# Optimization experiments

Hardware: AMD Instinct MI355X
Metric: run time of the kernel (lower is better)

The kernel has to match this reference:

```python
import jax, jax.numpy as jnp
import numpy as np

N_USERS = 100000
N_ITEMS = 50000
N_NODES = N_USERS + N_ITEMS  # 150000
N_EDGES = 1000000
N_INTENTS = 4
EMBED_K = 64
CHUNK = EMBED_K // N_INTENTS  # 16
N_LAYERS = 3


def setup_inputs() -> dict:
    key = jax.random.key(0)
    k1, k2, k3, k4 = jax.random.split(key, 4)
    Gu = jax.random.normal(k1, (N_USERS, EMBED_K), dtype=jnp.float32) * 0.1
    Gi = jax.random.normal(k2, (N_ITEMS, EMBED_K), dtype=jnp.float32) * 0.1
    edge_index = jax.random.randint(k3, (2, N_EDGES), 0, N_NODES, dtype=jnp.int64)
    edge_index_intents = jax.random.normal(k4, (N_INTENTS, N_EDGES), dtype=jnp.float32)
    return {"Gu": Gu, "Gi": Gi, "edge_index": edge_index,
            "edge_index_intents": edge_index_intents}


def dgcf_layer(x, row, col, edge_index_intents):
    # x: [N, K, C]; edge_index_intents: [K, E]
    w = jax.nn.softmax(edge_index_intents, axis=0).T  # [E, K]
    deg = (jax.ops.segment_sum(w, row, num_segments=N_NODES)
           + jax.ops.segment_sum(w, col, num_segments=N_NODES))  # [N, K]
    # deg^-0.5 with inf -> 0 (as in the torch code)
    dis = jnp.where(deg > 0, 1.0 / jnp.sqrt(jnp.maximum(deg, 1e-12)), 0.0)  # [N, K]
    norm = dis[row] * dis[col]  # [E, K]
    msg = norm[:, :, None] * x[row]  # [E, K, C] gather-multiply
    return jax.ops.segment_sum(msg, col, num_segments=N_NODES)  # scatter-add at targets


def reference(Gu, Gi, edge_index, edge_index_intents):
    row, col = edge_index[0], edge_index[1]
    # ego embeddings split into intent chunks: [N, K, C]
    x = jnp.concatenate([Gu, Gi], axis=0).reshape(N_NODES, N_INTENTS, CHUNK)
    for _ in range(N_LAYERS):
        x = dgcf_layer(x, row, col, edge_index_intents)
    return x
```

## Files before the change

### kernel.cpp

```cpp
#include <hip/hip_runtime.h>
#include <hip/hip_bf16.h>
#include <hip/hip_fp16.h>
#include <math.h>

#define N_USERS 100000
#define N_ITEMS 50000
#define N_NODES 150000
#define N_EDGES 1000000
#define N_GU_FLAT (N_USERS * 64)
#define N_ALL_FLAT (N_NODES * 64)
#define NBUCK 586
#define HPITCH (2 * NBUCK)
#define EPB 4096
#define NEB ((N_EDGES + EPB - 1) / EPB)
#define BCAP 2048
#define FIXS 16777216.0f
#define GCAST ((N_ALL_FLAT / 4 + 1023) / 1024)

typedef __hip_bfloat16 bf16;
typedef unsigned short ushort_t;
typedef unsigned int uint_t;
typedef unsigned long long u64_t;

__device__ __forceinline__ ushort_t f2bs(float f) {
    bf16 h = __float2bfloat16(f);
    return *reinterpret_cast<ushort_t*>(&h);
}
__device__ __forceinline__ float lo2f(uint_t u) {
    float f; *reinterpret_cast<uint_t*>(&f) = u << 16; return f;
}
__device__ __forceinline__ float hi2f(uint_t u) {
    float f; *reinterpret_cast<uint_t*>(&f) = u & 0xFFFF0000u; return f;
}
__device__ __forceinline__ uint_t pack2(float a, float b) {
    return (uint_t)f2bs(a) | ((uint_t)f2bs(b) << 16);
}
__device__ __forceinline__ ushort_t f2hs(float f) {
    __half h = __float2half(f);
    return *reinterpret_cast<ushort_t*>(&h);
}
__device__ __forceinline__ float hs2f(ushort_t u) {
    __half h; *reinterpret_cast<ushort_t*>(&h) = u;
    return __half2float(h);
}
__device__ __forceinline__ int fix24(float w) {
    return (int)__float2int_rn(w * FIXS);
}

__global__ __launch_bounds__(1024) void s3_scatter(
        const int* __restrict__ ei, const float* __restrict__ intents,
        uint_t* __restrict__ gctr,
        uint_t* __restrict__ tmp_meta, u64_t* __restrict__ tmp_w,
        u64_t* __restrict__ tmp_row) {
    extern __shared__ char smem[];
    u64_t*  cw    = (u64_t*)smem;
    u64_t*  rw    = (u64_t*)(smem + 32768);
    uint_t* cmeta = (uint_t*)(smem + 65536);
    uint_t* cpos  = (uint_t*)(smem + 81920);
    uint_t* rpos  = (uint_t*)(smem + 98304);
    uint_t* ctr   = (uint_t*)(smem + 114688);
    uint_t* lexcl = (uint_t*)(smem + 119376);
    uint_t* gb    = (uint_t*)(smem + 124064);
    uint_t* stmp  = cpos;
    int b = blockIdx.x, t = threadIdx.x;
    for (int j = t; j < HPITCH; j += 1024) ctr[j] = 0;
    __syncthreads();
    int eb = b * EPB;
    int lim = min(EPB, N_EDGES - eb);
    int  jcol[4], jrow[4];
    uint_t rkc[4], rkr[4], meta[4];
    u64_t cwv[4], rwv[4];
    bool val[4];
#pragma unroll
    for (int q = 0; q < 4; ++q) {
        int i = t + q * 1024;
        val[q] = (i < lim);
        int e = eb + (val[q] ? i : 0);
        int r = ei[e];
        int c = ei[N_EDGES + e];
        float v0 = intents[e];
        float v1 = intents[N_EDGES + e];
        float v2 = intents[2 * N_EDGES + e];
        float v3 = intents[3 * N_EDGES + e];
        float m  = fmaxf(fmaxf(v0, v1), fmaxf(v2, v3));
        float x0 = __expf(v0 - m), x1 = __expf(v1 - m);
        float x2 = __expf(v2 - m), x3 = __expf(v3 - m);
        float inv = 1.0f / (x0 + x1 + x2 + x3);
        float w0 = x0 * inv, w1 = x1 * inv, w2 = x2 * inv, w3 = x3 * inv;
        jcol[q] = c >> 8;
        jrow[q] = r >> 8;
        if (val[q]) {
            rkc[q] = atomicAdd(&ctr[jcol[q]], 1u);
            rkr[q] = atomicAdd(&ctr[NBUCK + jrow[q]], 1u);
        }
        meta[q] = ((uint_t)(c & 255) << 24) | (uint_t)r;
        cwv[q]  = (u64_t)pack2(w0, w1) | ((u64_t)pack2(w2, w3) << 32);
        rwv[q]  = (u64_t)f2hs(w0) | ((u64_t)f2hs(w1) << 16) |
                  ((u64_t)f2hs(w2) << 32) | ((u64_t)(uint_t)(r & 255) << 48);
    }
    __syncthreads();
    for (int j = t; j < HPITCH; j += 1024)
        gb[j] = atomicAdd(&gctr[j], ctr[j]);
    {
        uint_t v = (t < NBUCK) ? ctr[t] : 0u;
        stmp[t] = v;
        __syncthreads();
        for (int off = 1; off < 1024; off <<= 1) {
            uint_t a = (t >= off) ? stmp[t - off] : 0u;
            __syncthreads();
            stmp[t] += a;
            __syncthreads();
        }
        if (t < NBUCK) lexcl[t] = stmp[t] - v;
    }
    __syncthreads();
    {
        uint_t v = (t < NBUCK) ? ctr[NBUCK + t] : 0u;
        stmp[t] = v;
        __syncthreads();
        for (int off = 1; off < 1024; off <<= 1) {
            uint_t a = (t >= off) ? stmp[t - off] : 0u;
            __syncthreads();
            stmp[t] += a;
            __syncthreads();
        }
        if (t < NBUCK) lexcl[NBUCK + t] = stmp[t] - v;
    }
    __syncthreads();
#pragma unroll
    for (int q = 0; q < 4; ++q) {
        if (!val[q]) continue;
        uint_t lp = lexcl[jcol[q]] + rkc[q];
        cmeta[lp] = meta[q];
        cw[lp]    = cwv[q];
        cpos[lp]  = (uint_t)jcol[q] * BCAP + gb[jcol[q]] + rkc[q];
        uint_t lr = lexcl[NBUCK + jrow[q]] + rkr[q];
        rw[lr]    = rwv[q];
        rpos[lr]  = (uint_t)jrow[q] * BCAP + gb[NBUCK + jrow[q]] + rkr[q];
    }
    __syncthreads();
    for (int i = t; i < lim; i += 1024) {
        uint_t p = cpos[i];
        tmp_meta[p] = cmeta[i];
        tmp_w[p]    = cw[i];
        tmp_row[rpos[i]] = rw[i];
    }
}

__global__ __launch_bounds__(1024) void s4_finalize(
        const uint_t* __restrict__ tmp_meta, const u64_t* __restrict__ tmp_w,
        const u64_t* __restrict__ tmp_row, const uint_t* __restrict__ gctr,
        const float* __restrict__ Gu, const float* __restrict__ Gi,
        ushort_t* __restrict__ xG,
        uint_t* __restrict__ rec_src, int* __restrict__ offs_c, int* __restrict__ cnt_c,
        float* __restrict__ dis) {
    __shared__ uint_t meta_s[BCAP];
    __shared__ u64_t  w_s[BCAP];
    __shared__ u64_t  rw_s[BCAP];
    __shared__ uint_t hist[256], excl[256], run[256], sc[256];
    __shared__ int deg[1024];
    int b = blockIdx.x, t = threadIdx.x;
    if (b >= NBUCK) {
        long base = ((long)(b - NBUCK) * 1024 + t) * 4;
        if (base >= N_ALL_FLAT) return;
        float4 v = (base < N_GU_FLAT) ? *(const float4*)(Gu + base)
                                      : *(const float4*)(Gi + (base - N_GU_FLAT));
        uint2 o;
        o.x = pack2(v.x, v.y);
        o.y = pack2(v.z, v.w);
        *(uint2*)(xG + base) = o;
        return;
    }
    if (t < 256) { hist[t] = 0u; run[t] = 0u; }
    deg[t] = 0;
    __syncthreads();
    uint_t c0 = (uint_t)b * BCAP;
    int nc = min((int)gctr[b], BCAP);
    int nr = min((int)gctr[NBUCK + b], BCAP);
    for (int i = t; i < nc; i += 1024) {
        meta_s[i] = tmp_meta[c0 + i];
        w_s[i]    = tmp_w[c0 + i];
    }
    for (int i = t; i < nr; i += 1024) rw_s[i] = tmp_row[c0 + i];
    __syncthreads();
    for (int i = t; i < nc; i += 1024) {
        uint_t nl = meta_s[i] >> 24;
        u64_t w = w_s[i];
        atomicAdd(&hist[nl], 1u);
        atomicAdd(&deg[nl * 4 + 0], fix24(lo2f((uint_t)w)));
        atomicAdd(&deg[nl * 4 + 1], fix24(hi2f((uint_t)w)));
        atomicAdd(&deg[nl * 4 + 2], fix24(lo2f((uint_t)(w >> 32))));
        atomicAdd(&deg[nl * 4 + 3], fix24(hi2f((uint_t)(w >> 32))));
    }
    for (int i = t; i < nr; i += 1024) {
        u64_t rv = rw_s[i];
        uint_t nl = (uint_t)(rv >> 48) & 255u;
        float w0 = hs2f((ushort_t)(rv & 0xFFFF));
        float w1 = hs2f((ushort_t)((rv >> 16) & 0xFFFF));
        float w2 = hs2f((ushort_t)((rv >> 32) & 0xFFFF));
        float w3 = 1.0f - w0 - w1 - w2;
        atomicAdd(&deg[nl * 4 + 0], fix24(w0));
        atomicAdd(&deg[nl * 4 + 1], fix24(w1));
        atomicAdd(&deg[nl * 4 + 2], fix24(w2));
        atomicAdd(&deg[nl * 4 + 3], fix24(w3));
    }
    __syncthreads();
    if (t < 256) sc[t] = hist[t];
    __syncthreads();
    for (int off = 1; off < 256; off <<= 1) {
        uint_t a = (t < 256 && t >= off) ? sc[t - off] : 0u;
        __syncthreads();
        if (t < 256) sc[t] += a;
        __syncthreads();
    }
    if (t < 256) excl[t] = sc[t] - hist[t];
    __syncthreads();
    for (int i = t; i < nc; i += 1024) {
        uint_t m = meta_s[i];
        uint_t nl = m >> 24;
        uint_t p = atomicAdd(&run[nl], 1u);
        rec_src[c0 + excl[nl] + p] = m & 0x00FFFFFFu;
    }
    if (t < 256) {
        int n = b * 256 + t;
        if (n < N_NODES) {
            offs_c[n] = (int)(c0 + excl[t]);
            cnt_c[n]  = (int)hist[t];
            float d0 = (float)deg[t * 4 + 0] * (1.0f / FIXS);
            float d1 = (float)deg[t * 4 + 1] * (1.0f / FIXS);
            float d2 = (float)deg[t * 4 + 2] * (1.0f / FIXS);
            float d3 = (float)deg[t * 4 + 3] * (1.0f / FIXS);
            float4 dd;
            dd.x = (d0 > 0.f) ? rsqrtf(fmaxf(d0, 1e-12f)) : 0.f;
            dd.y = (d1 > 0.f) ? rsqrtf(fmaxf(d1, 1e-12f)) : 0.f;
            dd.z = (d2 > 0.f) ? rsqrtf(fmaxf(d2, 1e-12f)) : 0.f;
            dd.w = (d3 > 0.f) ? rsqrtf(fmaxf(d3, 1e-12f)) : 0.f;
            *(float4*)(dis + (size_t)n * 4) = dd;
        }
    }
}

template <int MODE>
__global__ __launch_bounds__(256) void dg_agg(const ushort_t* __restrict__ xin,
                                              ushort_t* __restrict__ xout_b,
                                              float* __restrict__ xout_f,
                                              const uint_t* __restrict__ rec_src,
                                              const int* __restrict__ cnt_c,
                                              const int* __restrict__ offs_c,
                                              const float* __restrict__ dis) {
    int n = (blockIdx.x * 256 + threadIdx.x) >> 3;
    if (n >= N_NODES) return;
    int lane = threadIdx.x & 63;
    int j = lane & 7, k = j >> 1;
    int sg = lane & 56;
    int base = offs_c[n];
    int cnt  = cnt_c[n];
    float dd = dis[n * 4 + k];
    float a0 = 0.f, a1 = 0.f, a2 = 0.f, a3 = 0.f;
    float a4 = 0.f, a5 = 0.f, a6 = 0.f, a7 = 0.f;
    for (int c = 0; c < cnt; c += 8) {
        int idx = c + j;
        uint_t sv = (idx < cnt) ? rec_src[base + idx] : 0u;
        int srcs[8];
#pragma unroll
        for (int i = 0; i < 8; ++i) srcs[i] = (int)__shfl(sv, sg + i, 64);
#pragma unroll
        for (int i = 0; i < 8; ++i) {
            bool v = (c + i) < cnt;
            int src = v ? srcs[i] : srcs[0];
            float nk = v ? ((MODE == 0) ? dis[src * 4 + k] : 1.f) : 0.f;
            uint4 xu = *(const uint4*)(xin + (long)src * 64 + j * 8);
            a0 = fmaf(nk, lo2f(xu.x), a0); a1 = fmaf(nk, hi2f(xu.x), a1);
            a2 = fmaf(nk, lo2f(xu.y), a2); a3 = fmaf(nk, hi2f(xu.y), a3);
            a4 = fmaf(nk, lo2f(xu.z), a4); a5 = fmaf(nk, hi2f(xu.z), a5);
            a6 = fmaf(nk, lo2f(xu.w), a6); a7 = fmaf(nk, hi2f(xu.w), a7);
        }
    }
    float sc = (MODE == 2) ? dd : dd * dd;
    a0 *= sc; a1 *= sc; a2 *= sc; a3 *= sc;
    a4 *= sc; a5 *= sc; a6 *= sc; a7 *= sc;
    long o = (long)n * 64 + j * 8;
    if (MODE == 2) {
        *(float4*)(xout_f + o)     = make_float4(a0, a1, a2, a3);
        *(float4*)(xout_f + o + 4) = make_float4(a4, a5, a6, a7);
    } else {
        uint4 ob;
        ob.x = pack2(a0, a1); ob.y = pack2(a2, a3);
        ob.z = pack2(a4, a5); ob.w = pack2(a6, a7);
        *(uint4*)(xout_b + o) = ob;
    }
}

extern "C" void kernel_launch(void* const* d_in, const int* in_sizes, int n_in,
                              void* d_out, int out_size, void* d_ws, size_t ws_size,
                              hipStream_t stream) {
    const float* Gu      = (const float*)d_in[0];
    const float* Gi      = (const float*)d_in[1];
    const int*   ei      = (const int*)d_in[2];
    const float* intents = (const float*)d_in[3];
    float* out = (float*)d_out;

    char* ws = (char*)d_ws;
    size_t off = 0;
    int* offs_c = (int*)(ws + off);       off += (size_t)N_NODES * 4;
    int* cnt_c  = (int*)(ws + off);       off += (size_t)N_NODES * 4;
    float* dis  = (float*)(ws + off);     off += (size_t)N_NODES * 16;
    uint_t* rec_src = (uint_t*)(ws + off); off += (size_t)NBUCK * BCAP * 4;
    uint_t* gctr    = (uint_t*)(ws + off); off += 8192;
    ushort_t* xG = (ushort_t*)(ws + off); off += (size_t)N_ALL_FLAT * 2;
    ushort_t* xA = (ushort_t*)(ws + off); off += (size_t)N_ALL_FLAT * 2;
    ushort_t* xB = (ushort_t*)(ws + off); off += (size_t)N_ALL_FLAT * 2;
    uint_t* tmp_meta = (uint_t*)xA;
    u64_t*  tmp_w    = (u64_t*)((char*)xA + (size_t)NBUCK * BCAP * 4);
    u64_t*  tmp_row  = (u64_t*)xB;
    (void)ws_size; (void)in_sizes; (void)n_in; (void)out_size;

    hipMemsetAsync(gctr, 0, HPITCH * sizeof(uint_t), stream);

    const size_t S3_LDS = 128752;
    hipFuncSetAttribute((const void*)s3_scatter,
                        hipFuncAttributeMaxDynamicSharedMemorySize, (int)S3_LDS);
    s3_scatter<<<NEB, 1024, S3_LDS, stream>>>(ei, intents, gctr,
                                              tmp_meta, tmp_w, tmp_row);
    s4_finalize<<<NBUCK + GCAST, 1024, 0, stream>>>(tmp_meta, tmp_w, tmp_row, gctr,
                                                    Gu, Gi, xG,
                                                    rec_src, offs_c, cnt_c, dis);

    int gAgg = (N_NODES * 8 + 255) / 256;
    dg_agg<0><<<gAgg, 256, 0, stream>>>(xG, xA, nullptr, rec_src, cnt_c, offs_c, dis);
    dg_agg<1><<<gAgg, 256, 0, stream>>>(xA, xB, nullptr, rec_src, cnt_c, offs_c, dis);
    dg_agg<2><<<gAgg, 256, 0, stream>>>(xB, nullptr, out, rec_src, cnt_c, offs_c, dis);
}
```

Measured before the change: 213.8 us.

## Prescale input by dis in finalize and use wave-shuffle bucket scans

```diff
diff --git a/kernel.cpp b/kernel.cpp
--- a/kernel.cpp
+++ b/kernel.cpp
@@ -10,12 +10,12 @@
 #define N_GU_FLAT (N_USERS * 64)
 #define N_ALL_FLAT (N_NODES * 64)
 #define NBUCK 586
-#define HPITCH (2 * NBUCK)
+#define BPITCH 1280
+#define ROWB 640
 #define EPB 4096
 #define NEB ((N_EDGES + EPB - 1) / EPB)
 #define BCAP 2048
 #define FIXS 16777216.0f
-#define GCAST ((N_ALL_FLAT / 4 + 1023) / 1024)
 
 typedef __hip_bfloat16 bf16;
 typedef unsigned short ushort_t;
@@ -59,11 +59,11 @@
     uint_t* cpos  = (uint_t*)(smem + 81920);
     uint_t* rpos  = (uint_t*)(smem + 98304);
     uint_t* ctr   = (uint_t*)(smem + 114688);
-    uint_t* lexcl = (uint_t*)(smem + 119376);
-    uint_t* gb    = (uint_t*)(smem + 124064);
-    uint_t* stmp  = cpos;
+    uint_t* lexcl = (uint_t*)(smem + 119808);
+    uint_t* gb    = (uint_t*)(smem + 124928);
+    uint_t* wtot  = (uint_t*)(smem + 130048);
     int b = blockIdx.x, t = threadIdx.x;
-    for (int j = t; j < HPITCH; j += 1024) ctr[j] = 0;
+    for (int j = t; j < BPITCH; j += 1024) ctr[j] = 0;
     __syncthreads();
     int eb = b * EPB;
     int lim = min(EPB, N_EDGES - eb);
@@ -91,7 +91,7 @@
         jrow[q] = r >> 8;
         if (val[q]) {
             rkc[q] = atomicAdd(&ctr[jcol[q]], 1u);
-            rkr[q] = atomicAdd(&ctr[NBUCK + jrow[q]], 1u);
+            rkr[q] = atomicAdd(&ctr[ROWB + jrow[q]], 1u);
         }
         meta[q] = ((uint_t)(c & 255) << 24) | (uint_t)r;
         cwv[q]  = (u64_t)pack2(w0, w1) | ((u64_t)pack2(w2, w3) << 32);
@@ -99,32 +99,40 @@
                   ((u64_t)f2hs(w2) << 32) | ((u64_t)(uint_t)(r & 255) << 48);
     }
     __syncthreads();
-    for (int j = t; j < HPITCH; j += 1024)
+    for (int j = t; j < BPITCH; j += 1024)
         gb[j] = atomicAdd(&gctr[j], ctr[j]);
     {
-        uint_t v = (t < NBUCK) ? ctr[t] : 0u;
-        stmp[t] = v;
-        __syncthreads();
-        for (int off = 1; off < 1024; off <<= 1) {
-            uint_t a = (t >= off) ? stmp[t - off] : 0u;
-            __syncthreads();
-            stmp[t] += a;
-            __syncthreads();
-        }
-        if (t < NBUCK) lexcl[t] = stmp[t] - v;
+        int wave = t >> 6, lane = t & 63;
+        for (int c = wave; c < 20; c += 16) {
+            uint_t v = ctr[c * 64 + lane];
+            uint_t x = v;
+#pragma unroll
+            for (int off = 1; off < 64; off <<= 1) {
+                uint_t u = __shfl_up(x, off, 64);
+                if (lane >= off) x += u;
+            }
+            lexcl[c * 64 + lane] = x - v;
+            if (lane == 63) wtot[c] = x;
+        }
+    }
+    __syncthreads();
+    if (t < 32) {
+        uint_t tv = (t < 20) ? wtot[t] : 0u;
+        uint_t x = tv;
+#pragma unroll
+        for (int off = 1; off < 32; off <<= 1) {
+            uint_t u = __shfl_up(x, off, 32);
+            if (t >= off) x += u;
+        }
+        uint_t colTot = __shfl(x, 9, 32);
+        uint_t base = x - tv - ((t >= 10) ? colTot : 0u);
+        if (t < 20) wtot[t] = base;
     }
     __syncthreads();
     {
-        uint_t v = (t < NBUCK) ? ctr[NBUCK + t] : 0u;
-        stmp[t] = v;
-        __syncthreads();
-        for (int off = 1; off < 1024; off <<= 1) {
-            uint_t a = (t >= off) ? stmp[t - off] : 0u;
-            __syncthreads();
-            stmp[t] += a;
-            __syncthreads();
-        }
-        if (t < NBUCK) lexcl[NBUCK + t] = stmp[t] - v;
+        int wave = t >> 6, lane = t & 63;
+        for (int c = wave; c < 20; c += 16)
+            lexcl[c * 64 + lane] += wtot[c];
     }
     __syncthreads();
 #pragma unroll
@@ -134,9 +142,9 @@
         cmeta[lp] = meta[q];
         cw[lp]    = cwv[q];
         cpos[lp]  = (uint_t)jcol[q] * BCAP + gb[jcol[q]] + rkc[q];
-        uint_t lr = lexcl[NBUCK + jrow[q]] + rkr[q];
+        uint_t lr = lexcl[ROWB + jrow[q]] + rkr[q];
         rw[lr]    = rwv[q];
-        rpos[lr]  = (uint_t)jrow[q] * BCAP + gb[NBUCK + jrow[q]] + rkr[q];
+        rpos[lr]  = (uint_t)jrow[q] * BCAP + gb[ROWB + jrow[q]] + rkr[q];
     }
     __syncthreads();
     for (int i = t; i < lim; i += 1024) {
@@ -151,7 +159,7 @@
         const uint_t* __restrict__ tmp_meta, const u64_t* __restrict__ tmp_w,
         const u64_t* __restrict__ tmp_row, const uint_t* __restrict__ gctr,
         const float* __restrict__ Gu, const float* __restrict__ Gi,
-        ushort_t* __restrict__ xG,
+        ushort_t* __restrict__ y0,
         uint_t* __restrict__ rec_src, int* __restrict__ offs_c, int* __restrict__ cnt_c,
         float* __restrict__ dis) {
     __shared__ uint_t meta_s[BCAP];
@@ -159,24 +167,14 @@
     __shared__ u64_t  rw_s[BCAP];
     __shared__ uint_t hist[256], excl[256], run[256], sc[256];
     __shared__ int deg[1024];
+    float* dis_s = (float*)deg;
     int b = blockIdx.x, t = threadIdx.x;
-    if (b >= NBUCK) {
-        long base = ((long)(b - NBUCK) * 1024 + t) * 4;
-        if (base >= N_ALL_FLAT) return;
-        float4 v = (base < N_GU_FLAT) ? *(const float4*)(Gu + base)
-                                      : *(const float4*)(Gi + (base - N_GU_FLAT));
-        uint2 o;
-        o.x = pack2(v.x, v.y);
-        o.y = pack2(v.z, v.w);
-        *(uint2*)(xG + base) = o;
-        return;
-    }
     if (t < 256) { hist[t] = 0u; run[t] = 0u; }
     deg[t] = 0;
     __syncthreads();
     uint_t c0 = (uint_t)b * BCAP;
     int nc = min((int)gctr[b], BCAP);
-    int nr = min((int)gctr[NBUCK + b], BCAP);
+    int nr = min((int)gctr[ROWB + b], BCAP);
     for (int i = t; i < nc; i += 1024) {
         meta_s[i] = tmp_meta[c0 + i];
         w_s[i]    = tmp_w[c0 + i];
@@ -236,11 +234,36 @@
             dd.z = (d2 > 0.f) ? rsqrtf(fmaxf(d2, 1e-12f)) : 0.f;
             dd.w = (d3 > 0.f) ? rsqrtf(fmaxf(d3, 1e-12f)) : 0.f;
             *(float4*)(dis + (size_t)n * 4) = dd;
-        }
-    }
-}
-
-template <int MODE>
+            dis_s[t * 4 + 0] = dd.x;
+            dis_s[t * 4 + 1] = dd.y;
+            dis_s[t * 4 + 2] = dd.z;
+            dis_s[t * 4 + 3] = dd.w;
+        }
+    }
+    __syncthreads();
+    {
+        int nl = t >> 2, q = t & 3;
+        int n = b * 256 + nl;
+        if (n < N_NODES) {
+            const float* g = (n < N_USERS) ? Gu + (size_t)n * 64 + q * 16
+                                           : Gi + (size_t)(n - N_USERS) * 64 + q * 16;
+            float s = dis_s[nl * 4 + q];
+            float4 v0 = *(const float4*)(g);
+            float4 v1 = *(const float4*)(g + 4);
+            float4 v2 = *(const float4*)(g + 8);
+            float4 v3 = *(const float4*)(g + 12);
+            uint4 o0, o1;
+            o0.x = pack2(v0.x * s, v0.y * s); o0.y = pack2(v0.z * s, v0.w * s);
+            o0.z = pack2(v1.x * s, v1.y * s); o0.w = pack2(v1.z * s, v1.w * s);
+            o1.x = pack2(v2.x * s, v2.y * s); o1.y = pack2(v2.z * s, v2.w * s);
+            o1.z = pack2(v3.x * s, v3.y * s); o1.w = pack2(v3.z * s, v3.w * s);
+            *(uint4*)(y0 + (size_t)n * 64 + q * 16)     = o0;
+            *(uint4*)(y0 + (size_t)n * 64 + q * 16 + 8) = o1;
+        }
+    }
+}
+
+template <int LAST>
 __global__ __launch_bounds__(256) void dg_agg(const ushort_t* __restrict__ xin,
                                               ushort_t* __restrict__ xout_b,
                                               float* __restrict__ xout_f,
@@ -268,7 +291,7 @@
         for (int i = 0; i < 8; ++i) {
             bool v = (c + i) < cnt;
             int src = v ? srcs[i] : srcs[0];
-            float nk = v ? ((MODE == 0) ? dis[src * 4 + k] : 1.f) : 0.f;
+            float nk = v ? 1.f : 0.f;
             uint4 xu = *(const uint4*)(xin + (long)src * 64 + j * 8);
             a0 = fmaf(nk, lo2f(xu.x), a0); a1 = fmaf(nk, hi2f(xu.x), a1);
             a2 = fmaf(nk, lo2f(xu.y), a2); a3 = fmaf(nk, hi2f(xu.y), a3);
@@ -276,11 +299,11 @@
             a6 = fmaf(nk, lo2f(xu.w), a6); a7 = fmaf(nk, hi2f(xu.w), a7);
         }
     }
-    float sc = (MODE == 2) ? dd : dd * dd;
+    float sc = LAST ? dd : dd * dd;
     a0 *= sc; a1 *= sc; a2 *= sc; a3 *= sc;
     a4 *= sc; a5 *= sc; a6 *= sc; a7 *= sc;
     long o = (long)n * 64 + j * 8;
-    if (MODE == 2) {
+    if (LAST) {
         *(float4*)(xout_f + o)     = make_float4(a0, a1, a2, a3);
         *(float4*)(xout_f + o + 4) = make_float4(a4, a5, a6, a7);
     } else {
@@ -315,19 +338,19 @@
     u64_t*  tmp_row  = (u64_t*)xB;
     (void)ws_size; (void)in_sizes; (void)n_in; (void)out_size;
 
-    hipMemsetAsync(gctr, 0, HPITCH * sizeof(uint_t), stream);
-
-    const size_t S3_LDS = 128752;
+    hipMemsetAsync(gctr, 0, BPITCH * sizeof(uint_t), stream);
+
+    const size_t S3_LDS = 130176;
     hipFuncSetAttribute((const void*)s3_scatter,
                         hipFuncAttributeMaxDynamicSharedMemorySize, (int)S3_LDS);
     s3_scatter<<<NEB, 1024, S3_LDS, stream>>>(ei, intents, gctr,
                                               tmp_meta, tmp_w, tmp_row);
-    s4_finalize<<<NBUCK + GCAST, 1024, 0, stream>>>(tmp_meta, tmp_w, tmp_row, gctr,
-                                                    Gu, Gi, xG,
-                                                    rec_src, offs_c, cnt_c, dis);
+    s4_finalize<<<NBUCK, 1024, 0, stream>>>(tmp_meta, tmp_w, tmp_row, gctr,
+                                            Gu, Gi, xG,
+                                            rec_src, offs_c, cnt_c, dis);
 
     int gAgg = (N_NODES * 8 + 255) / 256;
     dg_agg<0><<<gAgg, 256, 0, stream>>>(xG, xA, nullptr, rec_src, cnt_c, offs_c, dis);
-    dg_agg<1><<<gAgg, 256, 0, stream>>>(xA, xB, nullptr, rec_src, cnt_c, offs_c, dis);
-    dg_agg<2><<<gAgg, 256, 0, stream>>>(xB, nullptr, out, rec_src, cnt_c, offs_c, dis);
-}
+    dg_agg<0><<<gAgg, 256, 0, stream>>>(xA, xB, nullptr, rec_src, cnt_c, offs_c, dis);
+    dg_agg<1><<<gAgg, 256, 0, stream>>>(xB, nullptr, out, rec_src, cnt_c, offs_c, dis);
+}
```

New measurement: 211.0 us. No clear change (-1.3%).
